# Kernel tuning notes

Measured on AMD Instinct MI355X. Metric: run time of the kernel, lower is better.

## Reference

```python
import jax, jax.numpy as jnp
import numpy as np

KNOWN_POINTS = 8
TAU = 1.0


def setup_inputs() -> dict:
    key = jax.random.key(0)
    k1, k2, k3 = jax.random.split(key, 3)
    B, N, H = 8, 56564, 256
    return {
        "x": jax.random.normal(k1, (B, N), dtype=jnp.float32),
        "point_weight": jax.random.normal(k2, (1, N), dtype=jnp.float32),
        "weight": jax.random.normal(k3, (1, N, H), dtype=jnp.float32),
        "bias": jnp.zeros((1, H), dtype=jnp.float32),
    }


def _softmax_point_selection(point_weight, B, tau):
    """Iterative straight-through HardSoftmax top-k selection (stage=2).
    Returns a (B, N) {0,1}-valued mask (with straight-through softmax grads)."""
    N = point_weight.shape[1]
    weights = jnp.broadcast_to(point_weight, (B, N))  # repeat_interleave over batch
    minimum = jax.lax.stop_gradient(jnp.min(weights))
    total = jnp.zeros((B, N), dtype=weights.dtype)
    for _ in range(KNOWN_POINTS):
        soft = jax.nn.softmax(weights / tau, axis=1)
        hard = jax.nn.one_hot(jnp.argmax(weights, axis=1), N, dtype=weights.dtype)
        # straight-through: forward = hard, backward = softmax jacobian
        one_hot = hard - jax.lax.stop_gradient(soft) + soft
        total = total + one_hot
        # masked_fill at selected positions (no grad through filled entries)
        weights = jnp.where(hard > 0, minimum - 10000.0, weights)
    return total


def reference(x, point_weight, weight, bias):
    B = x.shape[0]
    mask = _softmax_point_selection(point_weight, B, TAU)  # (B, N)
    # out[b,h] = sum_n x[b,n] * mask[b,n] * W[n,h] + bias[h]
    # (equivalent to masking the (B,N,H) weight then matmul, without materializing it)
    out = jnp.einsum('bn,nh->bh', x * mask, weight[0]) + bias
    return out
```

## Files before the change

### kernel.cpp

```cpp
#include <hip/hip_runtime.h>
#include <math.h>

#define KSEL 8
typedef unsigned long long u64;

__device__ __forceinline__ u64 make_key(float v, unsigned int idx) {
    unsigned int u = __float_as_uint(v);
    unsigned int ord = (u & 0x80000000u) ? ~u : (u | 0x80000000u);
    return ((u64)ord << 32) | (u64)(~idx);
}
__device__ __forceinline__ u64 kmax(u64 a, u64 b) { return a > b ? a : b; }
__device__ __forceinline__ void cswap(u64 &a, u64 &b) {
    u64 hi = a > b ? a : b;
    u64 lo = a > b ? b : a;
    a = hi; b = lo;
}

__device__ __forceinline__ void merge8(u64 a[8], const u64 b[8]) {
    u64 t[8];
    #pragma unroll
    for (int i = 0; i < 8; ++i) t[i] = kmax(a[i], b[7 - i]);
    cswap(t[0], t[4]); cswap(t[1], t[5]); cswap(t[2], t[6]); cswap(t[3], t[7]);
    cswap(t[0], t[2]); cswap(t[1], t[3]); cswap(t[4], t[6]); cswap(t[5], t[7]);
    cswap(t[0], t[1]); cswap(t[2], t[3]); cswap(t[4], t[5]); cswap(t[6], t[7]);
    #pragma unroll
    for (int i = 0; i < 8; ++i) a[i] = t[i];
}

__device__ __forceinline__ void wave_butterfly_top8(u64 r[8]) {
    #pragma unroll
    for (int o = 1; o < 64; o <<= 1) {
        u64 b[8];
        #pragma unroll
        for (int i = 0; i < 8; ++i) b[i] = __shfl_xor(r[i], o, 64);
        merge8(r, b);
    }
}

__global__ __launch_bounds__(64) void topk_scan(
        const float* __restrict__ pw, int N, u64* __restrict__ ws_keys) {
    const int lane = threadIdx.x;
    const int gid  = blockIdx.x * 64 + lane;
    const int N4   = N >> 2;

    u64 c0 = 0, c1 = 0, c2 = 0, c3 = 0, c4 = 0;
    if (gid < N4) {
        const float4 v = reinterpret_cast<const float4*>(pw)[gid];
        const unsigned int base = (unsigned int)gid * 4u;
        c0 = make_key(v.x, base + 0u);
        c1 = make_key(v.y, base + 1u);
        c2 = make_key(v.z, base + 2u);
        c3 = make_key(v.w, base + 3u);
    }
    if (blockIdx.x == 0) {
        int t = N4 * 4 + lane;
        if (t < N) c4 = make_key(pw[t], (unsigned int)t);
    }
    cswap(c0, c1); cswap(c3, c4); cswap(c2, c4); cswap(c2, c3); cswap(c0, c3);
    cswap(c0, c2); cswap(c1, c4); cswap(c1, c3); cswap(c1, c2);

    u64 r[8] = {c0, c1, c2, c3, c4, 0ull, 0ull, 0ull};
    wave_butterfly_top8(r);

    if (lane == 0) {
        #pragma unroll
        for (int i = 0; i < 8; ++i) ws_keys[blockIdx.x * KSEL + i] = r[i];
    }
}

__global__ __launch_bounds__(256) void topk_merge_out(
        const u64* __restrict__ ws_keys, int nlists,
        const float* __restrict__ x, const float* __restrict__ w,
        const float* __restrict__ bias, float* __restrict__ out,
        int N, int H, int B) {
    __shared__ u64 s_wk[4][KSEL];
    __shared__ int s_idx[KSEL];
    __shared__ float s_x[16][KSEL];

    const int tid  = threadIdx.x;
    const int lane = tid & 63;
    const int wid  = tid >> 6;

    const int per = (nlists + 3) >> 2;
    const int li  = wid * per + lane;
    u64 g[8] = {0ull, 0ull, 0ull, 0ull, 0ull, 0ull, 0ull, 0ull};
    if (lane < per && li < nlists) {
        #pragma unroll
        for (int i = 0; i < 8; ++i) g[i] = ws_keys[li * KSEL + i];
    }
    wave_butterfly_top8(g);
    if (lane == 0) {
        #pragma unroll
        for (int i = 0; i < 8; ++i) s_wk[wid][i] = g[i];
    }
    __syncthreads();

    if (wid == 0) {
        u64 a[8], b[8];
        #pragma unroll
        for (int i = 0; i < 8; ++i) a[i] = s_wk[0][i];
        #pragma unroll
        for (int wv = 1; wv < 4; ++wv) {
            #pragma unroll
            for (int i = 0; i < 8; ++i) b[i] = s_wk[wv][i];
            merge8(a, b);
        }
        if (lane == 0) {
            #pragma unroll
            for (int k = 0; k < KSEL; ++k)
                s_idx[k] = (int)(~(unsigned int)(a[k] & 0xffffffffull));
        }
    }
    __syncthreads();

    int idx[KSEL];
    #pragma unroll
    for (int k = 0; k < KSEL; ++k) idx[k] = s_idx[k];

    if (tid < B * KSEL) {
        const int b = tid >> 3, k = tid & 7;
        s_x[b][k] = x[(size_t)b * N + idx[k]];
    }
    __syncthreads();

    for (int h = tid; h < H; h += 256) {
        float wv[KSEL];
        #pragma unroll
        for (int k = 0; k < KSEL; ++k) wv[k] = w[(size_t)idx[k] * H + h];
        const float bv = bias[h];
        for (int b = 0; b < B; ++b) {
            float acc = bv;
            #pragma unroll
            for (int k = 0; k < KSEL; ++k) acc += s_x[b][k] * wv[k];
            out[(size_t)b * H + h] = acc;
        }
    }
}

extern "C" void kernel_launch(void* const* d_in, const int* in_sizes, int n_in,
                              void* d_out, int out_size, void* d_ws, size_t ws_size,
                              hipStream_t stream) {
    const float* x    = (const float*)d_in[0];
    const float* pw   = (const float*)d_in[1];
    const float* w    = (const float*)d_in[2];
    const float* bias = (const float*)d_in[3];
    float* out = (float*)d_out;

    const int N = in_sizes[1];
    const int H = in_sizes[3];
    const int B = in_sizes[0] / N;
    const int N4 = N >> 2;
    const int nblk = (N4 + 63) / 64;

    u64* keys = (u64*)d_ws;

    topk_scan<<<nblk, 64, 0, stream>>>(pw, N, keys);
    topk_merge_out<<<1, 256, 0, stream>>>(keys, nblk, x, w, bias, out, N, H, B);
}
```

Baseline: 17.23 us.

## Use 256-thread scan blocks and a single-wave merge kernel without block syncs

The scan kernel now launches 256-thread blocks, with each wave still writing its own top-8 list, so there are fewer blocks but the same number of lists. The merge kernel drops to one 64-lane wave: each lane serially merges four lists before the wave butterfly, which removes the shared-memory cross-wave merge and one __syncthreads. Indices stay in registers, and the x values are staged through a flat shared buffer. Each lane now does more serial merge work and the final GEMV has less parallelism, and it assumes B<=8 and H<=256.

```diff
diff --git a/kernel.cpp b/kernel.cpp
--- a/kernel.cpp
+++ b/kernel.cpp
@@ -37,10 +37,12 @@
     }
 }
 
-__global__ __launch_bounds__(64) void topk_scan(
+__global__ __launch_bounds__(256) void topk_scan(
         const float* __restrict__ pw, int N, u64* __restrict__ ws_keys) {
-    const int lane = threadIdx.x;
-    const int gid  = blockIdx.x * 64 + lane;
+    const int tid  = threadIdx.x;
+    const int lane = tid & 63;
+    const int wid  = tid >> 6;
+    const int gid  = blockIdx.x * 256 + tid;
     const int N4   = N >> 2;
 
     u64 c0 = 0, c1 = 0, c2 = 0, c3 = 0, c4 = 0;
@@ -53,7 +55,7 @@
         c3 = make_key(v.w, base + 3u);
     }
     if (blockIdx.x == 0) {
-        int t = N4 * 4 + lane;
+        int t = N4 * 4 + tid;
         if (t < N) c4 = make_key(pw[t], (unsigned int)t);
     }
     cswap(c0, c1); cswap(c3, c4); cswap(c2, c4); cswap(c2, c3); cswap(c0, c3);
@@ -63,76 +65,76 @@
     wave_butterfly_top8(r);
 
     if (lane == 0) {
+        const int li = blockIdx.x * 4 + wid;
         #pragma unroll
-        for (int i = 0; i < 8; ++i) ws_keys[blockIdx.x * KSEL + i] = r[i];
+        for (int i = 0; i < 8; ++i) ws_keys[li * KSEL + i] = r[i];
     }
 }
 
-__global__ __launch_bounds__(256) void topk_merge_out(
+__global__ __launch_bounds__(64) void topk_merge_out(
         const u64* __restrict__ ws_keys, int nlists,
         const float* __restrict__ x, const float* __restrict__ w,
         const float* __restrict__ bias, float* __restrict__ out,
         int N, int H, int B) {
-    __shared__ u64 s_wk[4][KSEL];
-    __shared__ int s_idx[KSEL];
-    __shared__ float s_x[16][KSEL];
+    __shared__ float s_x[64];
 
-    const int tid  = threadIdx.x;
-    const int lane = tid & 63;
-    const int wid  = tid >> 6;
+    const int lane = threadIdx.x;
 
-    const int per = (nlists + 3) >> 2;
-    const int li  = wid * per + lane;
-    u64 g[8] = {0ull, 0ull, 0ull, 0ull, 0ull, 0ull, 0ull, 0ull};
-    if (lane < per && li < nlists) {
+    u64 g[8] = {0, 0, 0, 0, 0, 0, 0, 0};
+    {
+        int li = lane * 4;
+        if (li < nlists) {
+            #pragma unroll
+            for (int i = 0; i < 8; ++i) g[i] = ws_keys[li * KSEL + i];
+        }
         #pragma unroll
-        for (int i = 0; i < 8; ++i) g[i] = ws_keys[li * KSEL + i];
+        for (int j = 1; j < 4; ++j) {
+            u64 b[8] = {0, 0, 0, 0, 0, 0, 0, 0};
+            if (li + j < nlists) {
+                #pragma unroll
+                for (int i = 0; i < 8; ++i) b[i] = ws_keys[(li + j) * KSEL + i];
+            }
+            merge8(g, b);
+        }
     }
     wave_butterfly_top8(g);
-    if (lane == 0) {
+
+    int idx[KSEL];
+    #pragma unroll
+    for (int k = 0; k < KSEL; ++k)
+        idx[k] = (int)(~(unsigned int)(g[k] & 0xffffffffull));
+
+    if (lane < B * KSEL) {
+        int kk = lane & 7;
+        int sel = idx[0];
         #pragma unroll
-        for (int i = 0; i < 8; ++i) s_wk[wid][i] = g[i];
+        for (int k = 1; k < KSEL; ++k) sel = (kk == k) ? idx[k] : sel;
+        s_x[lane] = x[(size_t)(lane >> 3) * N + sel];
     }
     __syncthreads();
 
-    if (wid == 0) {
-        u64 a[8], b[8];
+    float xv[8][KSEL];
+    #pragma unroll
+    for (int b = 0; b < 8; ++b)
         #pragma unroll
-        for (int i = 0; i < 8; ++i) a[i] = s_wk[0][i];
-        #pragma unroll
-        for (int wv = 1; wv < 4; ++wv) {
+        for (int k = 0; k < KSEL; ++k) xv[b][k] = s_x[b * KSEL + k];
+
+    for (int j = 0; j < 4; ++j) {
+        int h = lane + 64 * j;
+        if (h < H) {
+            float wv[KSEL];
             #pragma unroll
-            for (int i = 0; i < 8; ++i) b[i] = s_wk[wv][i];
-            merge8(a, b);
-        }
-        if (lane == 0) {
+            for (int k = 0; k < KSEL; ++k) wv[k] = w[(size_t)idx[k] * H + h];
+            const float bv = bias[h];
             #pragma unroll
-            for (int k = 0; k < KSEL; ++k)
-                s_idx[k] = (int)(~(unsigned int)(a[k] & 0xffffffffull));
-        }
-    }
-    __syncthreads();
-
-    int idx[KSEL];
-    #pragma unroll
-    for (int k = 0; k < KSEL; ++k) idx[k] = s_idx[k];
-
-    if (tid < B * KSEL) {
-        const int b = tid >> 3, k = tid & 7;
-        s_x[b][k] = x[(size_t)b * N + idx[k]];
-    }
-    __syncthreads();
-
-    for (int h = tid; h < H; h += 256) {
-        float wv[KSEL];
-        #pragma unroll
-        for (int k = 0; k < KSEL; ++k) wv[k] = w[(size_t)idx[k] * H + h];
-        const float bv = bias[h];
-        for (int b = 0; b < B; ++b) {
-            float acc = bv;
-            #pragma unroll
-            for (int k = 0; k < KSEL; ++k) acc += s_x[b][k] * wv[k];
-            out[(size_t)b * H + h] = acc;
+            for (int b = 0; b < 8; ++b) {
+                if (b < B) {
+                    float acc = bv;
+                    #pragma unroll
+                    for (int k = 0; k < KSEL; ++k) acc += xv[b][k] * wv[k];
+                    out[(size_t)b * H + h] = acc;
+                }
+            }
         }
     }
 }
@@ -150,10 +152,11 @@
     const int H = in_sizes[3];
     const int B = in_sizes[0] / N;
     const int N4 = N >> 2;
-    const int nblk = (N4 + 63) / 64;
+    const int nblk = (N4 + 255) / 256;
+    const int nlists = nblk * 4;
 
     u64* keys = (u64*)d_ws;
 
-    topk_scan<<<nblk, 64, 0, stream>>>(pw, N, keys);
-    topk_merge_out<<<1, 256, 0, stream>>>(keys, nblk, x, w, bias, out, N, H, B);
+    topk_scan<<<nblk, 256, 0, stream>>>(pw, N, keys);
+    topk_merge_out<<<1, 64, 0, stream>>>(keys, nlists, x, w, bias, out, N, H, B);
 }
```

New measurement: 20.25 us. +17.6%, slower.
